# Optimization experiments

Measured on AMD Instinct MI355X. Metric: run time of the kernel, lower is better.

## Reference

```python
import jax, jax.numpy as jnp
import numpy as np


def setup_inputs() -> dict:
    key = jax.random.key(0)
    k1, k2, k3 = jax.random.split(key, 3)
    dim = 192
    x = jax.random.normal(k1, (4, dim, 256, 256), dtype=jnp.float32)
    # Conv2d(5*dim, dim, 1): weight [dim, 5*dim], bias [dim]
    W = jax.random.normal(k2, (dim, 5 * dim), dtype=jnp.float32) * 0.02
    b = jax.random.normal(k3, (dim,), dtype=jnp.float32) * 0.02
    return {"x": x, "W": W, "b": b}


def _shifts(x):
    # Matches torch: cat([x,
    #   pad(x[:,:,:,1:], (0,1)),   # take right neighbor (zero at last col)
    #   pad(x[:,:,:,:-1], (1,0)),  # take left neighbor (zero at first col)
    #   pad(x[:,:,1:,:], (0,0,0,1)),  # take below neighbor (zero at last row)
    #   pad(x[:,:,:-1,:], (0,0,1,0))  # take above neighbor (zero at first row)
    # ], dim=1)
    right = jnp.pad(x[:, :, :, 1:], ((0, 0), (0, 0), (0, 0), (0, 1)))
    left = jnp.pad(x[:, :, :, :-1], ((0, 0), (0, 0), (0, 0), (1, 0)))
    down = jnp.pad(x[:, :, 1:, :], ((0, 0), (0, 0), (0, 1), (0, 0)))
    up = jnp.pad(x[:, :, :-1, :], ((0, 0), (0, 0), (1, 0), (0, 0)))
    return jnp.concatenate([x, right, left, down, up], axis=1)  # [B, 5C, H, W]


def reference(x, W, b):
    xs = _shifts(x)  # [B, 5C, H, W]
    # 1x1 conv == per-pixel matmul over channels
    out = jnp.einsum("bchw,oc->bohw", xs, W) + b[None, :, None, None]
    return out
```

## Files before the change

### kernel.cpp

```cpp
#include <hip/hip_runtime.h>
#include <hip/hip_bf16.h>
#include <stdint.h>

#define CDIM 192
#define KDIM 960
#define HW   65536
#define WI   256

#define OFF_BIAS 368640u
#define OFF_FLAG 369408u
#define NEED_WS  369472u

#define ROW_B    80
#define SLICE_B  10560
#define WOFF     31680
#define WBUF     12288

typedef __attribute__((ext_vector_type(8))) short short8;
typedef __attribute__((ext_vector_type(4))) float floatx4;

__device__ __forceinline__ uint16_t f2b(float v) {
    __hip_bfloat16 h = __float2bfloat16(v);
    return *reinterpret_cast<uint16_t*>(&h);
}

__global__ __launch_bounds__(256) void detect_kernel(const uint32_t* __restrict__ xw,
                                                     int* __restrict__ flag) {
    __shared__ int cnt;
    if (threadIdx.x == 0) cnt = 0;
    __syncthreads();
    int local = 0;
    #pragma unroll
    for (int i = 0; i < 4; ++i) {
        int s = threadIdx.x * 4 + i;
        uint32_t d = xw[(size_t)s * 24571];
        uint32_t e = (d >> 7) & 0xFF;
        if (e >= 110 && e <= 130) ++local;
    }
    atomicAdd(&cnt, local);
    __syncthreads();
    if (threadIdx.x == 0) *flag = (cnt >= 512) ? 1 : 0;
}

__global__ __launch_bounds__(256) void prep_kernel(const void* __restrict__ Wsrc,
                                                   const void* __restrict__ bsrc,
                                                   __hip_bfloat16* __restrict__ Wb,
                                                   float* __restrict__ bfp,
                                                   const int* __restrict__ flag) {
    const int f = *flag;
    if (blockIdx.x < 720) {
        int i = blockIdx.x * 256 + threadIdx.x;
        float v = f ? __bfloat162float(((const __hip_bfloat16*)Wsrc)[i])
                    : ((const float*)Wsrc)[i];
        Wb[i] = __float2bfloat16(v);
    } else if (threadIdx.x < CDIM) {
        int j = threadIdx.x;
        bfp[j] = f ? __bfloat162float(((const __hip_bfloat16*)bsrc)[j])
                   : ((const float*)bsrc)[j];
    }
}

__device__ __forceinline__ void gload16(const void* g, void* l) {
    __builtin_amdgcn_global_load_lds(
        (const __attribute__((address_space(1))) uint32_t*)g,
        (__attribute__((address_space(3))) uint32_t*)l, 16, 0, 0);
}

__global__ __launch_bounds__(256, 2) void fused_kernel(const void* __restrict__ xsrc,
                                                       const __hip_bfloat16* __restrict__ Wm,
                                                       const float* __restrict__ biasf,
                                                       void* __restrict__ outv,
                                                       const int* __restrict__ flag) {
    __shared__ char lds[WOFF + 2 * WBUF];
    char* xsl  = lds;
    char* ldsW = lds + WOFF;
    const int f = *flag;
    const int tid  = threadIdx.x;
    const int lane = tid & 63, wave = tid >> 6;
    const int quad = lane >> 4, l15 = lane & 15;

    const int nwg  = (int)gridDim.x;
    const int bid0 = (int)blockIdx.x;
    const int wg   = (bid0 & 7) * (nwg >> 3) + (bid0 >> 3);

    const int bb = wg >> 9;
    const int r  = wg & 511;
    const int h  = r >> 1;
    const int w0 = (r & 1) << 7;
    const int p0 = h * WI + w0;
    const int obase = (wave >> 1) * 96;
    const int nbase = (wave & 1) * 64;

    const char* gw[3];
    int ldsoff[3];
    #pragma unroll
    for (int t = 0; t < 3; ++t) {
        int chunk = tid + t * 256;
        int kq = chunk / 192, o = chunk % 192;
        gw[t] = (const char*)Wm + ((size_t)o * KDIM + kq * 8) * 2;
        ldsoff[t] = chunk * 16;
    }
    int aoff[6];
    #pragma unroll
    for (int mt = 0; mt < 6; ++mt) {
        int o = obase + mt * 16 + l15;
        aoff[mt] = (quad * 192 + o) * 16;
    }

    int pxa[4]; bool w255[4], wzero[4];
    #pragma unroll
    for (int nt = 0; nt < 4; ++nt) {
        int pl = nbase + nt * 16 + l15;
        pxa[nt]   = (pl + 1) * ROW_B;
        w255[nt]  = ((w0 + pl) == 255);
        wzero[nt] = ((w0 + pl) == 0);
    }

    const int scc  = tid >> 7;
    const int spx  = (tid & 127) + 1;
    const int scol = w0 + (tid & 127);
    const int ec = tid >> 1, ee = tid & 1;
    int ecol = ee ? (w0 + 128) : (w0 - 1);
    if (ecol < 0) ecol = 0;
    if (ecol > 255) ecol = 255;
    const int epx = ee ? 129 : 0;

    const size_t esz = f ? 2u : 4u;
    const char* xp = (const char*)xsrc + (size_t)bb * CDIM * HW * esz;

    int hr[3];
    #pragma unroll
    for (int rr = 0; rr < 3; ++rr) {
        int v = h - 1 + rr;
        hr[rr] = v < 0 ? 0 : (v > 255 ? 255 : v);
    }

    floatx4 acc[6][4];
    #pragma unroll
    for (int mt = 0; mt < 6; ++mt)
        #pragma unroll
        for (int nt = 0; nt < 4; ++nt)
            acc[mt][nt] = (floatx4){0.f, 0.f, 0.f, 0.f};

#define STAGE(JJ)                                                                          \
    {                                                                                      \
        const int c0 = (JJ) * 32;                                                          \
        _Pragma("unroll")                                                                  \
        for (int rr = 0; rr < 3; ++rr) {                                                   \
            uint32_t tmp[16];                                                              \
            const size_t rowoff = (size_t)hr[rr] * WI;                                     \
            if (f) {                                                                       \
                const uint16_t* xg = (const uint16_t*)xp;                                  \
                _Pragma("unroll")                                                          \
                for (int cc = 0; cc < 16; ++cc)                                            \
                    tmp[cc] = xg[(size_t)(c0 + scc * 16 + cc) * HW + rowoff + scol];       \
            } else {                                                                       \
                const float* xg = (const float*)xp;                                        \
                _Pragma("unroll")                                                          \
                for (int cc = 0; cc < 16; ++cc)                                            \
                    tmp[cc] = f2b(xg[(size_t)(c0 + scc * 16 + cc) * HW + rowoff + scol]);  \
            }                                                                              \
            uint4 q0, q1;                                                                  \
            q0.x = tmp[0] | (tmp[1] << 16);  q0.y = tmp[2] | (tmp[3] << 16);               \
            q0.z = tmp[4] | (tmp[5] << 16);  q0.w = tmp[6] | (tmp[7] << 16);               \
            q1.x = tmp[8] | (tmp[9] << 16);  q1.y = tmp[10] | (tmp[11] << 16);             \
            q1.z = tmp[12] | (tmp[13] << 16); q1.w = tmp[14] | (tmp[15] << 16);            \
            char* base = xsl + rr * SLICE_B + spx * ROW_B + scc * 32;                      \
            *(uint4*)(base)      = q0;                                                     \
            *(uint4*)(base + 16) = q1;                                                     \
        }                                                                                  \
        if (tid < 64) {                                                                    \
            _Pragma("unroll")                                                              \
            for (int rr = 0; rr < 3; ++rr) {                                               \
                const size_t gi = (size_t)(c0 + ec) * HW + (size_t)hr[rr] * WI + ecol;     \
                uint16_t v = f ? ((const uint16_t*)xp)[gi]                                 \
                               : f2b(((const float*)xp)[gi]);                              \
                *(uint16_t*)(xsl + rr * SLICE_B + epx * ROW_B + ec * 2) = v;               \
            }                                                                              \
        }                                                                                  \
    }

    #pragma unroll
    for (int t = 0; t < 3; ++t) gload16(gw[t], ldsW + ldsoff[t]);
    STAGE(0)
    __syncthreads();

    for (int j = 0; j < 6; ++j) {
        #pragma unroll
        for (int s = 0; s < 5; ++s) {
            const int cur = (s & 1) * WBUF;
            __builtin_amdgcn_s_barrier();
            __builtin_amdgcn_sched_barrier(0);
            if (s < 4) {
                const int nxt = WBUF - cur;
                #pragma unroll
                for (int t = 0; t < 3; ++t)
                    gload16(gw[t] + (size_t)((s + 1) * 6 + j) * 64, ldsW + nxt + ldsoff[t]);
            }
            __builtin_amdgcn_sched_barrier(0);
            if (s < 4) asm volatile("s_waitcnt vmcnt(3)" ::: "memory");
            else       asm volatile("s_waitcnt vmcnt(0)" ::: "memory");
            __builtin_amdgcn_sched_barrier(0);
            __builtin_amdgcn_s_barrier();
            __builtin_amdgcn_sched_barrier(0);

            short8 af[6];
            #pragma unroll
            for (int mt = 0; mt < 6; ++mt)
                af[mt] = *(const short8*)(ldsW + cur + aoff[mt]);

            const int so   = (s == 3) ? 2 * SLICE_B : (s == 4) ? 0 : SLICE_B;
            const int dw80 = (s == 1) ? ROW_B : (s == 2) ? -ROW_B : 0;
            const bool skip = (s == 3 && h == 255) || (s == 4 && h == 0);
            short8 bf[4];
            #pragma unroll
            for (int nt = 0; nt < 4; ++nt) {
                short8 v = *(const short8*)(xsl + so + pxa[nt] + dw80 + quad * 16);
                const bool kill = skip || (s == 1 && w255[nt]) || (s == 2 && wzero[nt]);
                bf[nt] = kill ? (short8){0, 0, 0, 0, 0, 0, 0, 0} : v;
            }

            __builtin_amdgcn_s_setprio(1);
            #pragma unroll
            for (int mt = 0; mt < 6; ++mt)
                #pragma unroll
                for (int nt = 0; nt < 4; ++nt)
                    acc[mt][nt] = __builtin_amdgcn_mfma_f32_16x16x32_bf16(
                        af[mt], bf[nt], acc[mt][nt], 0, 0, 0);
            __builtin_amdgcn_s_setprio(0);
        }
        if (j < 5) {
            __syncthreads();
            #pragma unroll
            for (int t = 0; t < 3; ++t)
                gload16(gw[t] + (size_t)(j + 1) * 64, ldsW + ldsoff[t]);
            STAGE(j + 1)
            __syncthreads();
        }
    }

    #pragma unroll
    for (int mt = 0; mt < 6; ++mt) {
        int o0 = obase + mt * 16 + quad * 4;
        float bv[4];
        #pragma unroll
        for (int rr = 0; rr < 4; ++rr) bv[rr] = biasf[o0 + rr];
        #pragma unroll
        for (int nt = 0; nt < 4; ++nt) {
            int px = nbase + nt * 16 + l15;
            size_t base = ((size_t)(bb * CDIM + o0) * HW) + p0 + px;
            if (f) {
                __hip_bfloat16* out = (__hip_bfloat16*)outv;
                #pragma unroll
                for (int rr = 0; rr < 4; ++rr)
                    out[base + (size_t)rr * HW] = __float2bfloat16(acc[mt][nt][rr] + bv[rr]);
            } else {
                float* out = (float*)outv;
                #pragma unroll
                for (int rr = 0; rr < 4; ++rr)
                    out[base + (size_t)rr * HW] = acc[mt][nt][rr] + bv[rr];
            }
        }
    }
#undef STAGE
}

__global__ __launch_bounds__(256) void fallback_kernel(const void* __restrict__ xv,
                                                       const void* __restrict__ Wv,
                                                       const void* __restrict__ bv,
                                                       void* __restrict__ outv,
                                                       const int* __restrict__ flag) {
    __shared__ float Wl[KDIM];
    const int f = *flag;
    const int tid = threadIdx.x;
    const int bid = blockIdx.x;
    const int h = bid & 255;
    const int bo = bid >> 8;
    const int o = bo % CDIM;
    const int b = bo / CDIM;
    if (f) {
        const __hip_bfloat16* W16 = (const __hip_bfloat16*)Wv;
        for (int i = tid; i < KDIM; i += 256) Wl[i] = __bfloat162float(W16[(size_t)o * KDIM + i]);
    } else {
        const float* W32 = (const float*)Wv;
        for (int i = tid; i < KDIM; i += 256) Wl[i] = W32[(size_t)o * KDIM + i];
    }
    __syncthreads();
    const size_t pb = (size_t)b * CDIM * HW + (size_t)h * WI + tid;
    float acc = f ? __bfloat162float(((const __hip_bfloat16*)bv)[o]) : ((const float*)bv)[o];
    if (f) {
        const __hip_bfloat16* x = (const __hip_bfloat16*)xv;
        for (int c = 0; c < CDIM; ++c) {
            const __hip_bfloat16* xp = x + pb + (size_t)c * HW;
            float ctr = __bfloat162float(xp[0]);
            float rgt = (tid < 255) ? __bfloat162float(xp[1])   : 0.f;
            float lft = (tid > 0)   ? __bfloat162float(xp[-1])  : 0.f;
            float dwn = (h < 255)   ? __bfloat162float(xp[WI])  : 0.f;
            float up  = (h > 0)     ? __bfloat162float(xp[-WI]) : 0.f;
            acc += ctr * Wl[c] + rgt * Wl[192 + c] + lft * Wl[384 + c]
                 + dwn * Wl[576 + c] + up * Wl[768 + c];
        }
    } else {
        const float* x = (const float*)xv;
        for (int c = 0; c < CDIM; ++c) {
            const float* xp = x + pb + (size_t)c * HW;
            float ctr = xp[0];
            float rgt = (tid < 255) ? xp[1]   : 0.f;
            float lft = (tid > 0)   ? xp[-1]  : 0.f;
            float dwn = (h < 255)   ? xp[WI]  : 0.f;
            float up  = (h > 0)     ? xp[-WI] : 0.f;
            acc += ctr * Wl[c] + rgt * Wl[192 + c] + lft * Wl[384 + c]
                 + dwn * Wl[576 + c] + up * Wl[768 + c];
        }
    }
    size_t oidx = (size_t)bo * HW + (size_t)h * WI + tid;
    if (f) ((__hip_bfloat16*)outv)[oidx] = __float2bfloat16(acc);
    else   ((float*)outv)[oidx] = acc;
}

extern "C" void kernel_launch(void* const* d_in, const int* in_sizes, int n_in,
                              void* d_out, int out_size, void* d_ws, size_t ws_size,
                              hipStream_t stream) {
    const uint32_t* xw = (const uint32_t*)d_in[0];
    char* ws = (char*)d_ws;

    if (ws_size >= NEED_WS) {
        __hip_bfloat16* Wb = (__hip_bfloat16*)ws;
        float* bfp = (float*)(ws + OFF_BIAS);
        int* flag  = (int*)(ws + OFF_FLAG);
        detect_kernel<<<1, 256, 0, stream>>>(xw, flag);
        prep_kernel<<<721, 256, 0, stream>>>(d_in[1], d_in[2], Wb, bfp, flag);
        fused_kernel<<<2048, 256, 0, stream>>>(d_in[0], Wb, bfp, d_out, flag);
    } else {
        int* flag = (int*)ws;
        detect_kernel<<<1, 256, 0, stream>>>(xw, flag);
        fallback_kernel<<<4 * CDIM * 256, 256, 0, stream>>>(d_in[0], d_in[1], d_in[2],
                                                            d_out, flag);
    }
}
```

Measured before the change: 464.0 us.

## Load weight fragments directly from global memory instead of staging through LDS

Drops the double-buffered LDS staging of weight tiles (global_load_lds plus barriers and waitcnt). Each wave now reads its A fragments straight from global memory, where they should stay cache-resident. This frees about 24KB of LDS and removes per-step barriers, so launch bounds go from 2 to 4 blocks per CU for more occupancy. In exchange, weight loads now have global/L2 latency on the MFMA critical path and are not prefetched ahead.

```diff
diff --git a/kernel.cpp b/kernel.cpp
--- a/kernel.cpp
+++ b/kernel.cpp
@@ -13,8 +13,7 @@
 
 #define ROW_B    80
 #define SLICE_B  10560
-#define WOFF     31680
-#define WBUF     12288
+#define LDS_TOT  31680
 
 typedef __attribute__((ext_vector_type(8))) short short8;
 typedef __attribute__((ext_vector_type(4))) float floatx4;
@@ -60,20 +59,12 @@
     }
 }
 
-__device__ __forceinline__ void gload16(const void* g, void* l) {
-    __builtin_amdgcn_global_load_lds(
-        (const __attribute__((address_space(1))) uint32_t*)g,
-        (__attribute__((address_space(3))) uint32_t*)l, 16, 0, 0);
-}
-
-__global__ __launch_bounds__(256, 2) void fused_kernel(const void* __restrict__ xsrc,
+__global__ __launch_bounds__(256, 4) void fused_kernel(const void* __restrict__ xsrc,
                                                        const __hip_bfloat16* __restrict__ Wm,
                                                        const float* __restrict__ biasf,
                                                        void* __restrict__ outv,
                                                        const int* __restrict__ flag) {
-    __shared__ char lds[WOFF + 2 * WBUF];
-    char* xsl  = lds;
-    char* ldsW = lds + WOFF;
+    __shared__ char xsl[LDS_TOT];
     const int f = *flag;
     const int tid  = threadIdx.x;
     const int lane = tid & 63, wave = tid >> 6;
@@ -91,20 +82,11 @@
     const int obase = (wave >> 1) * 96;
     const int nbase = (wave & 1) * 64;
 
-    const char* gw[3];
-    int ldsoff[3];
-    #pragma unroll
-    for (int t = 0; t < 3; ++t) {
-        int chunk = tid + t * 256;
-        int kq = chunk / 192, o = chunk % 192;
-        gw[t] = (const char*)Wm + ((size_t)o * KDIM + kq * 8) * 2;
-        ldsoff[t] = chunk * 16;
-    }
-    int aoff[6];
+    const char* wbase[6];
     #pragma unroll
     for (int mt = 0; mt < 6; ++mt) {
         int o = obase + mt * 16 + l15;
-        aoff[mt] = (quad * 192 + o) * 16;
+        wbase[mt] = (const char*)Wm + (size_t)o * (KDIM * 2) + quad * 16;
     }
 
     int pxa[4]; bool w255[4], wzero[4];
@@ -180,34 +162,16 @@
         }                                                                                  \
     }
 
-    #pragma unroll
-    for (int t = 0; t < 3; ++t) gload16(gw[t], ldsW + ldsoff[t]);
     STAGE(0)
     __syncthreads();
 
     for (int j = 0; j < 6; ++j) {
         #pragma unroll
         for (int s = 0; s < 5; ++s) {
-            const int cur = (s & 1) * WBUF;
-            __builtin_amdgcn_s_barrier();
-            __builtin_amdgcn_sched_barrier(0);
-            if (s < 4) {
-                const int nxt = WBUF - cur;
-                #pragma unroll
-                for (int t = 0; t < 3; ++t)
-                    gload16(gw[t] + (size_t)((s + 1) * 6 + j) * 64, ldsW + nxt + ldsoff[t]);
-            }
-            __builtin_amdgcn_sched_barrier(0);
-            if (s < 4) asm volatile("s_waitcnt vmcnt(3)" ::: "memory");
-            else       asm volatile("s_waitcnt vmcnt(0)" ::: "memory");
-            __builtin_amdgcn_sched_barrier(0);
-            __builtin_amdgcn_s_barrier();
-            __builtin_amdgcn_sched_barrier(0);
-
             short8 af[6];
             #pragma unroll
             for (int mt = 0; mt < 6; ++mt)
-                af[mt] = *(const short8*)(ldsW + cur + aoff[mt]);
+                af[mt] = *(const short8*)(wbase[mt] + (size_t)(s * 6 + j) * 64);
 
             const int so   = (s == 3) ? 2 * SLICE_B : (s == 4) ? 0 : SLICE_B;
             const int dw80 = (s == 1) ? ROW_B : (s == 2) ? -ROW_B : 0;
@@ -231,9 +195,6 @@
         }
         if (j < 5) {
             __syncthreads();
-            #pragma unroll
-            for (int t = 0; t < 3; ++t)
-                gload16(gw[t] + (size_t)(j + 1) * 64, ldsW + ldsoff[t]);
             STAGE(j + 1)
             __syncthreads();
         }
```

Result: slower. 1.116 ms (+140.5%).
